# Optimization experiments

Measured on AMD Instinct MI355X. Metric: run time of the kernel, lower is better.

Reference implementation:

```python
import jax, jax.numpy as jnp
import numpy as np

# ---- config (from init_kwargs) ----
IMG_SIZE = (4096.0, 4096.0)
MAP_SIZE = (256, 256)
BASE_SIZE = 16
RATIOS = np.array([0.5, 1.0, 2.0], dtype=np.float64)
SCALES = np.array([8.0, 16.0, 32.0], dtype=np.float64)
FEAT_STRIDE = 16
RPN_MIN_SIZE = 16.0
PRE_NMS_N = 12000
POST_NMS_N = 2000
NMS_THRESH = 0.7


def _generate_anchors():
    base = np.array([1, 1, BASE_SIZE, BASE_SIZE], dtype=np.float64) - 1
    w = base[2] - base[0] + 1
    h = base[3] - base[1] + 1
    cx = base[0] + 0.5 * (w - 1)
    cy = base[1] + 0.5 * (h - 1)
    size = w * h
    ws = np.round(np.sqrt(size / RATIOS))
    hs = np.round(ws * RATIOS)
    ratio_anchors = np.stack([cx - 0.5 * (ws - 1), cy - 0.5 * (hs - 1),
                              cx + 0.5 * (ws - 1), cy + 0.5 * (hs - 1)], axis=1)
    out = []
    for a in ratio_anchors:
        aw = a[2] - a[0] + 1
        ah = a[3] - a[1] + 1
        acx = a[0] + 0.5 * (aw - 1)
        acy = a[1] + 0.5 * (ah - 1)
        ws2 = aw * SCALES
        hs2 = ah * SCALES
        out.append(np.stack([acx - 0.5 * (ws2 - 1), acy - 0.5 * (hs2 - 1),
                             acx + 0.5 * (ws2 - 1), acy + 0.5 * (hs2 - 1)], axis=1))
    return np.concatenate(out, axis=0).astype(np.float32)  # [A=9, 4]


def _all_anchors():
    A = _generate_anchors()
    H, W = MAP_SIZE
    sx = np.arange(W) * FEAT_STRIDE
    sy = np.arange(H) * FEAT_STRIDE
    sx, sy = np.meshgrid(sx, sy)
    shifts = np.stack([sx.ravel(), sy.ravel(), sx.ravel(), sy.ravel()], axis=1).astype(np.float32)  # [K,4]
    return (shifts[:, None, :] + A[None, :, :]).reshape(-1, 4)  # [K*A, 4]


_ALL_ANCHORS = _all_anchors()  # [N, 4] constant


def setup_inputs() -> dict:
    key = jax.random.key(0)
    k1, k2 = jax.random.split(key)
    n = _ALL_ANCHORS.shape[0]
    delta = jax.random.normal(k1, (1, n, 4), dtype=jnp.float32) * 0.1
    score = jax.random.uniform(k2, (1, n, 2), dtype=jnp.float32)
    return {"delta": delta, "score": score}


def _proposal_forward(delta, score):
    anchors = jnp.asarray(_ALL_ANCHORS)  # [N,4]
    d = delta[0]                         # [N,4]
    s = score[0, :, 1]                   # [N]

    widths = anchors[:, 2] - anchors[:, 0] + 1.0
    heights = anchors[:, 3] - anchors[:, 1] + 1.0
    ctr_x = anchors[:, 0] + 0.5 * widths
    ctr_y = anchors[:, 1] + 0.5 * heights
    pcx = d[:, 0] * widths + ctr_x
    pcy = d[:, 1] * heights + ctr_y
    pw = jnp.exp(d[:, 2]) * widths
    ph = jnp.exp(d[:, 3]) * heights
    x0 = jnp.clip(pcx - 0.5 * pw, 0.0, IMG_SIZE[0])
    y0 = jnp.clip(pcy - 0.5 * ph, 0.0, IMG_SIZE[1])
    x1 = jnp.clip(pcx + 0.5 * pw, 0.0, IMG_SIZE[0])
    y1 = jnp.clip(pcy + 0.5 * ph, 0.0, IMG_SIZE[1])
    props = jnp.stack([x0, y0, x1, y1], axis=1)  # [N,4]

    # min-size filter: mask instead of dynamic gather (jit-friendly)
    w = props[:, 2] - props[:, 0]
    h = props[:, 3] - props[:, 1]
    valid = (w >= RPN_MIN_SIZE) & (h >= RPN_MIN_SIZE)
    s = jnp.where(valid, s, -jnp.inf)

    top_s, top_i = jax.lax.top_k(s, PRE_NMS_N)   # sorted descending
    boxes = props[top_i]                          # [PRE,4]

    # greedy NMS over score-sorted boxes, fixed POST_NMS_N iterations
    areas = (boxes[:, 2] - boxes[:, 0]) * (boxes[:, 3] - boxes[:, 1])
    alive0 = top_s > -jnp.inf

    def step(alive, _):
        i = jnp.argmax(jnp.where(alive, top_s, -jnp.inf))
        ok = alive[i]
        b = boxes[i]
        xx0 = jnp.maximum(b[0], boxes[:, 0])
        yy0 = jnp.maximum(b[1], boxes[:, 1])
        xx1 = jnp.minimum(b[2], boxes[:, 2])
        yy1 = jnp.minimum(b[3], boxes[:, 3])
        inter = jnp.maximum(xx1 - xx0, 0.0) * jnp.maximum(yy1 - yy0, 0.0)
        iou = inter / jnp.maximum(areas[i] + areas - inter, 1e-8)
        alive = alive & (iou <= NMS_THRESH)
        out = jnp.where(ok, b, jnp.zeros_like(b))  # zero-pad like tf.pad
        return alive, out

    _, selected = jax.lax.scan(step, alive0, None, length=POST_NMS_N)  # [POST,4]
    return selected[None]  # [1, POST_NMS_N, 4]


def reference(delta, score):
    return _proposal_forward(delta, score)
```

## Files before the change

kernel.cpp:

```cpp
#include <hip/hip_runtime.h>
#include <hip/hip_bf16.h>

#define N_ANCH   589824
#define NBLK     2304
#define TOPK     12000
#define KPAD     12032
#define NW       188
#define OUTN     2000
#define CAP      32768

typedef unsigned long long u64;

__constant__ float c_aw[9] = {184.f, 368.f, 736.f, 128.f, 256.f, 512.f,  88.f, 176.f, 352.f};
__constant__ float c_ah[9] = { 96.f, 192.f, 384.f, 128.f, 256.f, 512.f, 176.f, 352.f, 704.f};

__device__ __forceinline__ void decode_one(int i, const float4* __restrict__ delta,
                                           float4* box, bool* valid) {
#pragma clang fp contract(off)
    int a    = i % 9;
    int cell = i / 9;
    int gx = cell & 255;
    int gy = cell >> 8;
    float w = c_aw[a], h = c_ah[a];
    float cx = (float)gx * 16.0f + 8.0f;
    float cy = (float)gy * 16.0f + 8.0f;
    float4 d = delta[i];
    float pcx = d.x * w + cx;
    float pcy = d.y * h + cy;
    float pw  = expf(d.z) * w;
    float ph  = expf(d.w) * h;
    float x0 = fminf(fmaxf(pcx - 0.5f * pw, 0.f), 4096.f);
    float y0 = fminf(fmaxf(pcy - 0.5f * ph, 0.f), 4096.f);
    float x1 = fminf(fmaxf(pcx + 0.5f * pw, 0.f), 4096.f);
    float y1 = fminf(fmaxf(pcy + 0.5f * ph, 0.f), 4096.f);
    *box = make_float4(x0, y0, x1, y1);
    *valid = (x1 - x0 >= 16.f) && (y1 - y0 >= 16.f);
}

__global__ __launch_bounds__(256) void k_score(const float4* __restrict__ delta,
                                               const float2* __restrict__ score,
                                               unsigned* __restrict__ ukey,
                                               unsigned* __restrict__ hist1) {
    __shared__ unsigned lh[256];
    int tid = threadIdx.x;
    lh[tid] = 0u;
    __syncthreads();
    int i = blockIdx.x * 256 + tid;
    float4 box; bool valid;
    decode_one(i, delta, &box, &valid);
    unsigned u = 0u;
    if (valid) {
        unsigned b = __float_as_uint(score[i].y);
        u = (b & 0x80000000u) ? ~b : (b | 0x80000000u);
    }
    ukey[i] = u;
    atomicAdd(&lh[u >> 24], 1u);
    __syncthreads();
    unsigned c = lh[tid];
    if (c) atomicAdd(&hist1[tid], c);
}

__global__ __launch_bounds__(256) void k_hist2(const unsigned* __restrict__ ukey,
                                               const unsigned* __restrict__ hist1,
                                               unsigned* __restrict__ hist2) {
    __shared__ unsigned ss[256];
    __shared__ unsigned lh[256];
    __shared__ unsigned s_b1;
    int tid = threadIdx.x;
    ss[tid] = hist1[tid];
    lh[tid] = 0u;
    if (tid == 0) s_b1 = 0u;
    __syncthreads();
    for (int d = 1; d < 256; d <<= 1) {
        unsigned v = (tid + d < 256) ? ss[tid + d] : 0u;
        __syncthreads();
        ss[tid] += v;
        __syncthreads();
    }
    if (ss[tid] >= (unsigned)TOPK && (tid == 255 || ss[tid + 1] < (unsigned)TOPK))
        s_b1 = (unsigned)tid;
    __syncthreads();
    unsigned b1 = s_b1;
    int i = blockIdx.x * 256 + tid;
    unsigned u = ukey[i];
    if ((u >> 24) == b1) atomicAdd(&lh[(u >> 16) & 255u], 1u);
    __syncthreads();
    unsigned c = lh[tid];
    if (c) atomicAdd(&hist2[tid], c);
}

__global__ __launch_bounds__(256) void k_compact(const unsigned* __restrict__ ukey,
                                                 const unsigned* __restrict__ hist1,
                                                 const unsigned* __restrict__ hist2,
                                                 unsigned* __restrict__ cnt,
                                                 u64* __restrict__ cand) {
    __shared__ unsigned ss[256];
    __shared__ unsigned s_b1, s_ab1, s_P;
    int tid = threadIdx.x;
    ss[tid] = hist1[tid];
    if (tid == 0) { s_b1 = 0u; s_ab1 = 0u; }
    __syncthreads();
    for (int d = 1; d < 256; d <<= 1) {
        unsigned v = (tid + d < 256) ? ss[tid + d] : 0u;
        __syncthreads();
        ss[tid] += v;
        __syncthreads();
    }
    if (ss[tid] >= (unsigned)TOPK && (tid == 255 || ss[tid + 1] < (unsigned)TOPK)) {
        s_b1 = (unsigned)tid;
        s_ab1 = (tid == 255) ? 0u : ss[tid + 1];
    }
    __syncthreads();
    unsigned b1 = s_b1, ab1 = s_ab1;
    ss[tid] = hist2[tid];
    if (tid == 0) s_P = (b1 << 8);
    __syncthreads();
    for (int d = 1; d < 256; d <<= 1) {
        unsigned v = (tid + d < 256) ? ss[tid + d] : 0u;
        __syncthreads();
        ss[tid] += v;
        __syncthreads();
    }
    unsigned target = (unsigned)TOPK - ab1;
    if (ss[tid] >= target && (tid == 255 || ss[tid + 1] < target))
        s_P = (b1 << 8) | (unsigned)tid;
    __syncthreads();
    unsigned P = s_P;

    int i = blockIdx.x * 256 + tid;
    unsigned u = ukey[i];
    bool pred = (u != 0u) && ((u >> 16) >= P);
    u64 m = __ballot(pred);
    if (m == 0ull) return;
    int lane = tid & 63;
    int leader = __ffsll(m) - 1;
    unsigned base = 0;
    if (lane == leader) base = atomicAdd(cnt, (unsigned)__popcll(m));
    base = __shfl(base, leader);
    if (pred) {
        u64 below = m & ((1ull << lane) - 1ull);
        unsigned pos = base + (unsigned)__popcll(below);
        if (pos < CAP) cand[pos] = ((u64)u << 32) | (unsigned)(~i);
    }
}

__global__ __launch_bounds__(256) void k_rankdec(const u64* __restrict__ cand,
                                                 const unsigned* __restrict__ ctrl,
                                                 const float4* __restrict__ delta,
                                                 float4* __restrict__ sboxes) {
    unsigned cnt = ctrl[3];
    int C = (int)(cnt < (unsigned)CAP ? cnt : (unsigned)CAP);
    if ((int)(blockIdx.x * 256) >= C) return;
    int t = blockIdx.x * 256 + threadIdx.x;
    u64 mykey = (t < C) ? cand[t] : ~0ull;
    int rank = 0;
    __shared__ u64 tile[256];
    for (int j0 = 0; j0 < C; j0 += 256) {
        int j = j0 + threadIdx.x;
        tile[threadIdx.x] = (j < C) ? cand[j] : 0ull;
        __syncthreads();
        int lim = (C - j0 < 256) ? (C - j0) : 256;
        #pragma unroll 4
        for (int jj = 0; jj < lim; ++jj) rank += (tile[jj] > mykey) ? 1 : 0;
        __syncthreads();
    }
    if (t < C && rank < TOPK) {
        int idx = (int)(~(unsigned)mykey);
        float4 box; bool v;
        decode_one(idx, delta, &box, &v);
        sboxes[rank] = box;
    }
}

__global__ __launch_bounds__(64) void k_mask(const float4* __restrict__ sboxes,
                                             u64* __restrict__ mcol) {
    int rb = blockIdx.y;
    int cb0 = blockIdx.x * 4;
    if (cb0 + 3 < rb) return;
    int tid = threadIdx.x;
    int r = rb * 64 + tid;
    float4 me = sboxes[r];
    float areaMe = (me.z - me.x) * (me.w - me.y);
    __shared__ float4 cbox[64];
    for (int q = 0; q < 4; ++q) {
        int cb = cb0 + q;
        if (cb < rb) continue;
        __syncthreads();
        cbox[tid] = sboxes[cb * 64 + tid];
        __syncthreads();
        u64 bits = 0ull;
        for (int j = 0; j < 64; ++j) {
            float4 o = cbox[j];
            float xx0 = fmaxf(me.x, o.x);
            float yy0 = fmaxf(me.y, o.y);
            float xx1 = fminf(me.z, o.z);
            float yy1 = fminf(me.w, o.w);
            float iw = fmaxf(xx1 - xx0, 0.f);
            float ih = fmaxf(yy1 - yy0, 0.f);
            float inter = iw * ih;
            float areaO = (o.z - o.x) * (o.w - o.y);
            float denom = fmaxf(areaMe + areaO - inter, 1e-8f);
            float iou = inter / denom;
            if (iou > 0.7f && (cb * 64 + j) != r) bits |= (1ull << j);
        }
        mcol[(size_t)cb * KPAD + r] = bits;
    }
}

__global__ __launch_bounds__(256) void k_reduce(const float4* __restrict__ sboxes,
                                                const unsigned* __restrict__ ctrl,
                                                const u64* __restrict__ mcol,
                                                float4* __restrict__ out) {
    int t = threadIdx.x;
    int lane = t & 63;
    int wave = t >> 6;
    unsigned cnt = ctrl[3];
    int C = (int)(cnt < (unsigned)CAP ? cnt : (unsigned)CAP);
    int nvalid = C < TOPK ? C : TOPK;
    int nblocks = (nvalid + 63) >> 6;

    __shared__ u64 s_rw[2];

    u64 removed_t = ~0ull;
    if (t < NW) {
        long long lo = (long long)t * 64;
        if (lo + 64 <= (long long)nvalid) removed_t = 0ull;
        else if (lo < (long long)nvalid)
            removed_t = ~((1ull << (unsigned)(nvalid - lo)) - 1ull);
    }

    int nk = 0;
    u64 p0=0,p1=0,p2=0,p3=0,p4=0,p5=0,p6=0,p7=0;
    u64 p8=0,p9=0,p10=0,p11=0,p12=0,p13=0,p14=0,p15=0;
    u64 dgnext = 0ull;
    if (nblocks > 0) dgnext = mcol[(size_t)0 * KPAD + lane];

    for (int b = 0; b < nblocks; ++b) {
        removed_t |= ((p0|p1)|(p2|p3)) | ((p4|p5)|(p6|p7));
        removed_t |= ((p8|p9)|(p10|p11)) | ((p12|p13)|(p14|p15));
        p0=p1=p2=p3=p4=p5=p6=p7=0ull;
        p8=p9=p10=p11=p12=p13=p14=p15=0ull;
        u64 dg = dgnext;
        if (t == b) s_rw[b & 1] = removed_t;
        __syncthreads();
        u64 rw = s_rw[b & 1];
        if (b + 1 < nblocks)
            dgnext = mcol[(size_t)(b + 1) * KPAD + (size_t)(b + 1) * 64 + lane];

        bool alive = ((rw >> lane) & 1ull) == 0ull;
        int budget = OUTN - nk;
        u64 keptmask = 0ull;
        int kc = 0;
        while (kc < budget) {
            u64 m = __ballot(alive);
            if (!m) break;
            int j = __ffsll(m) - 1;
            keptmask |= (1ull << j);
            ++kc;
            alive = alive && (lane != j) && (((dg >> j) & 1ull) == 0ull);
        }

        if (wave == 0 && ((keptmask >> lane) & 1ull)) {
            int pos = nk + (int)__popcll(keptmask & ((1ull << lane) - 1ull));
            out[pos] = sboxes[b * 64 + lane];
        }
        nk += kc;
        if (nk >= OUTN) break;

        if (kc > 0 && t > b && t < NW) {
            const u64* colp = mcol + (size_t)t * KPAD + (size_t)b * 64;
            u64 km = keptmask;
            int jf = __ffsll(km) - 1;
            int i0 = jf;                          km &= km - 1;
            int i1  = km ? __ffsll(km) - 1 : jf;  km &= km - 1;
            int i2  = km ? __ffsll(km) - 1 : jf;  km &= km - 1;
            int i3  = km ? __ffsll(km) - 1 : jf;  km &= km - 1;
            int i4  = km ? __ffsll(km) - 1 : jf;  km &= km - 1;
            int i5  = km ? __ffsll(km) - 1 : jf;  km &= km - 1;
            int i6  = km ? __ffsll(km) - 1 : jf;  km &= km - 1;
            int i7  = km ? __ffsll(km) - 1 : jf;  km &= km - 1;
            int i8  = km ? __ffsll(km) - 1 : jf;  km &= km - 1;
            int i9  = km ? __ffsll(km) - 1 : jf;  km &= km - 1;
            int i10 = km ? __ffsll(km) - 1 : jf;  km &= km - 1;
            int i11 = km ? __ffsll(km) - 1 : jf;  km &= km - 1;
            int i12 = km ? __ffsll(km) - 1 : jf;  km &= km - 1;
            int i13 = km ? __ffsll(km) - 1 : jf;  km &= km - 1;
            int i14 = km ? __ffsll(km) - 1 : jf;  km &= km - 1;
            int i15 = km ? __ffsll(km) - 1 : jf;  km &= km - 1;
            p0 = colp[i0];   p1 = colp[i1];   p2 = colp[i2];   p3 = colp[i3];
            p4 = colp[i4];   p5 = colp[i5];   p6 = colp[i6];   p7 = colp[i7];
            p8 = colp[i8];   p9 = colp[i9];   p10 = colp[i10]; p11 = colp[i11];
            p12 = colp[i12]; p13 = colp[i13]; p14 = colp[i14]; p15 = colp[i15];
            while (km) {
                int j = __ffsll(km) - 1; km &= km - 1;
                removed_t |= colp[j];
            }
        }
    }

    float4 z = make_float4(0.f, 0.f, 0.f, 0.f);
    for (int p = nk + t; p < OUTN; p += 256) out[p] = z;
}

extern "C" void kernel_launch(void* const* d_in, const int* in_sizes, int n_in,
                              void* d_out, int out_size, void* d_ws, size_t ws_size,
                              hipStream_t stream) {
    const float4* delta = (const float4*)d_in[0];
    const float2* score = (const float2*)d_in[1];
    char* ws = (char*)d_ws;

    unsigned* ukey  = (unsigned*)(ws + 0);
    u64*      cand  = (u64*)(ws + 2359296);
    unsigned* hist1 = (unsigned*)(ws + 2621440);
    unsigned* hist2 = (unsigned*)(ws + 2622464);
    unsigned* ctrl  = (unsigned*)(ws + 2623488);
    float4*   sbox  = (float4*)(ws + 2623552);
    u64*      mcol  = (u64*)(ws + 2816064);

    hipMemsetAsync(ws + 2621440, 0, 194624, stream);

    k_score  <<<NBLK,    256, 0, stream>>>(delta, score, ukey, hist1);
    k_hist2  <<<NBLK,    256, 0, stream>>>(ukey, hist1, hist2);
    k_compact<<<NBLK,    256, 0, stream>>>(ukey, hist1, hist2, ctrl + 3, cand);
    k_rankdec<<<CAP/256, 256, 0, stream>>>(cand, ctrl, delta, sbox);
    dim3 mgrid(47, NW);
    k_mask   <<<mgrid,   64,  0, stream>>>(sbox, mcol);
    k_reduce <<<1,       256, 0, stream>>>(sbox, ctrl, mcol, (float4*)d_out);
}
```

Before: 891.0 us.

## Single-pass 8192-bin histogram select, row-major mask, and pipelined NMS reduce

The two-level radix histogram (hist1 plus hist2) is replaced by a single 13-bit histogram accumulated in shared memory over grid-stride loops, which removes one full pass over the keys. The NMS mask is stored row-major with separate diagonal and superdiagonal arrays, and padded boxes are zeroed. The serial reduce now double-buffers the suppression-row loads and applies superdiagonal suppression through shared memory, aiming to shorten its critical path. In exchange, the 32 KB shared histogram may limit occupancy, and the row-major mask gathers are strided across threads.

```diff
diff --git a/kernel.cpp b/kernel.cpp
--- a/kernel.cpp
+++ b/kernel.cpp
@@ -1,13 +1,12 @@
 #include <hip/hip_runtime.h>
-#include <hip/hip_bf16.h>
 
 #define N_ANCH   589824
-#define NBLK     2304
 #define TOPK     12000
 #define KPAD     12032
 #define NW       188
 #define OUTN     2000
 #define CAP      32768
+#define NBIN     8192
 
 typedef unsigned long long u64;
 
@@ -40,36 +39,46 @@
 __global__ __launch_bounds__(256) void k_score(const float4* __restrict__ delta,
                                                const float2* __restrict__ score,
                                                unsigned* __restrict__ ukey,
-                                               unsigned* __restrict__ hist1) {
-    __shared__ unsigned lh[256];
+                                               unsigned* __restrict__ hist) {
+    __shared__ unsigned lh[NBIN];
     int tid = threadIdx.x;
-    lh[tid] = 0u;
+    for (int k = tid; k < NBIN; k += 256) lh[k] = 0u;
     __syncthreads();
-    int i = blockIdx.x * 256 + tid;
-    float4 box; bool valid;
-    decode_one(i, delta, &box, &valid);
-    unsigned u = 0u;
-    if (valid) {
-        unsigned b = __float_as_uint(score[i].y);
-        u = (b & 0x80000000u) ? ~b : (b | 0x80000000u);
-    }
-    ukey[i] = u;
-    atomicAdd(&lh[u >> 24], 1u);
+    for (int i = blockIdx.x * 256 + tid; i < N_ANCH; i += gridDim.x * 256) {
+        float4 box; bool valid;
+        decode_one(i, delta, &box, &valid);
+        unsigned u = 0u;
+        if (valid) {
+            unsigned b = __float_as_uint(score[i].y);
+            u = (b & 0x80000000u) ? ~b : (b | 0x80000000u);
+        }
+        ukey[i] = u;
+        atomicAdd(&lh[u >> 19], 1u);
+    }
     __syncthreads();
-    unsigned c = lh[tid];
-    if (c) atomicAdd(&hist1[tid], c);
-}
-
-__global__ __launch_bounds__(256) void k_hist2(const unsigned* __restrict__ ukey,
-                                               const unsigned* __restrict__ hist1,
-                                               unsigned* __restrict__ hist2) {
+    for (int k = tid; k < NBIN; k += 256) {
+        unsigned c = lh[k];
+        if (c) atomicAdd(&hist[k], c);
+    }
+}
+
+__global__ __launch_bounds__(256) void k_compact(const unsigned* __restrict__ ukey,
+                                                 const unsigned* __restrict__ hist,
+                                                 unsigned* __restrict__ cnt,
+                                                 u64* __restrict__ cand) {
     __shared__ unsigned ss[256];
-    __shared__ unsigned lh[256];
-    __shared__ unsigned s_b1;
+    __shared__ unsigned s_B;
     int tid = threadIdx.x;
-    ss[tid] = hist1[tid];
-    lh[tid] = 0u;
-    if (tid == 0) s_b1 = 0u;
+    int lane = tid & 63;
+    const uint4* hb = (const uint4*)hist + tid * 8;
+    unsigned cs = 0;
+    #pragma unroll
+    for (int k = 0; k < 8; ++k) {
+        uint4 h = hb[k];
+        cs += h.x + h.y + h.z + h.w;
+    }
+    ss[tid] = cs;
+    if (tid == 0) s_B = 0u;
     __syncthreads();
     for (int d = 1; d < 256; d <<= 1) {
         unsigned v = (tid + d < 256) ? ss[tid + d] : 0u;
@@ -77,70 +86,32 @@
         ss[tid] += v;
         __syncthreads();
     }
-    if (ss[tid] >= (unsigned)TOPK && (tid == 255 || ss[tid + 1] < (unsigned)TOPK))
-        s_b1 = (unsigned)tid;
+    if (ss[tid] >= (unsigned)TOPK && (tid == 255 || ss[tid + 1] < (unsigned)TOPK)) {
+        unsigned acc = (tid == 255) ? 0u : ss[tid + 1];
+        unsigned B = (unsigned)(tid * 32);
+        for (int j = 31; j >= 0; --j) {
+            acc += hist[tid * 32 + j];
+            if (acc >= (unsigned)TOPK) { B = (unsigned)(tid * 32 + j); break; }
+        }
+        s_B = B;
+    }
     __syncthreads();
-    unsigned b1 = s_b1;
-    int i = blockIdx.x * 256 + tid;
-    unsigned u = ukey[i];
-    if ((u >> 24) == b1) atomicAdd(&lh[(u >> 16) & 255u], 1u);
-    __syncthreads();
-    unsigned c = lh[tid];
-    if (c) atomicAdd(&hist2[tid], c);
-}
-
-__global__ __launch_bounds__(256) void k_compact(const unsigned* __restrict__ ukey,
-                                                 const unsigned* __restrict__ hist1,
-                                                 const unsigned* __restrict__ hist2,
-                                                 unsigned* __restrict__ cnt,
-                                                 u64* __restrict__ cand) {
-    __shared__ unsigned ss[256];
-    __shared__ unsigned s_b1, s_ab1, s_P;
-    int tid = threadIdx.x;
-    ss[tid] = hist1[tid];
-    if (tid == 0) { s_b1 = 0u; s_ab1 = 0u; }
-    __syncthreads();
-    for (int d = 1; d < 256; d <<= 1) {
-        unsigned v = (tid + d < 256) ? ss[tid + d] : 0u;
-        __syncthreads();
-        ss[tid] += v;
-        __syncthreads();
-    }
-    if (ss[tid] >= (unsigned)TOPK && (tid == 255 || ss[tid + 1] < (unsigned)TOPK)) {
-        s_b1 = (unsigned)tid;
-        s_ab1 = (tid == 255) ? 0u : ss[tid + 1];
-    }
-    __syncthreads();
-    unsigned b1 = s_b1, ab1 = s_ab1;
-    ss[tid] = hist2[tid];
-    if (tid == 0) s_P = (b1 << 8);
-    __syncthreads();
-    for (int d = 1; d < 256; d <<= 1) {
-        unsigned v = (tid + d < 256) ? ss[tid + d] : 0u;
-        __syncthreads();
-        ss[tid] += v;
-        __syncthreads();
-    }
-    unsigned target = (unsigned)TOPK - ab1;
-    if (ss[tid] >= target && (tid == 255 || ss[tid + 1] < target))
-        s_P = (b1 << 8) | (unsigned)tid;
-    __syncthreads();
-    unsigned P = s_P;
-
-    int i = blockIdx.x * 256 + tid;
-    unsigned u = ukey[i];
-    bool pred = (u != 0u) && ((u >> 16) >= P);
-    u64 m = __ballot(pred);
-    if (m == 0ull) return;
-    int lane = tid & 63;
-    int leader = __ffsll(m) - 1;
-    unsigned base = 0;
-    if (lane == leader) base = atomicAdd(cnt, (unsigned)__popcll(m));
-    base = __shfl(base, leader);
-    if (pred) {
-        u64 below = m & ((1ull << lane) - 1ull);
-        unsigned pos = base + (unsigned)__popcll(below);
-        if (pos < CAP) cand[pos] = ((u64)u << 32) | (unsigned)(~i);
+    unsigned B = s_B;
+    for (int i = blockIdx.x * 256 + tid; i < N_ANCH; i += gridDim.x * 256) {
+        unsigned u = ukey[i];
+        bool pred = (u != 0u) && ((u >> 19) >= B);
+        u64 m = __ballot(pred);
+        if (m) {
+            int leader = __ffsll(m) - 1;
+            unsigned base = 0;
+            if (lane == leader) base = atomicAdd(cnt, (unsigned)__popcll(m));
+            base = __shfl(base, leader);
+            if (pred) {
+                u64 below = m & ((1ull << lane) - 1ull);
+                unsigned pos = base + (unsigned)__popcll(below);
+                if (pos < CAP) cand[pos] = ((u64)u << 32) | (unsigned)(~i);
+            }
+        }
     }
 }
 
@@ -150,8 +121,10 @@
                                                  float4* __restrict__ sboxes) {
     unsigned cnt = ctrl[3];
     int C = (int)(cnt < (unsigned)CAP ? cnt : (unsigned)CAP);
+    int nv = C < TOPK ? C : TOPK;
+    int t = blockIdx.x * 256 + threadIdx.x;
+    if (t >= nv && t < KPAD) sboxes[t] = make_float4(0.f, 0.f, 0.f, 0.f);
     if ((int)(blockIdx.x * 256) >= C) return;
-    int t = blockIdx.x * 256 + threadIdx.x;
     u64 mykey = (t < C) ? cand[t] : ~0ull;
     int rank = 0;
     __shared__ u64 tile[256];
@@ -173,7 +146,8 @@
 }
 
 __global__ __launch_bounds__(64) void k_mask(const float4* __restrict__ sboxes,
-                                             u64* __restrict__ mcol) {
+                                             u64* __restrict__ mask,
+                                             u64* __restrict__ dgsd) {
     int rb = blockIdx.y;
     int cb0 = blockIdx.x * 4;
     if (cb0 + 3 < rb) return;
@@ -203,49 +177,105 @@
             float iou = inter / denom;
             if (iou > 0.7f && (cb * 64 + j) != r) bits |= (1ull << j);
         }
-        mcol[(size_t)cb * KPAD + r] = bits;
-    }
-}
+        mask[(size_t)r * NW + cb] = bits;
+        if (cb == rb)     dgsd[2 * r]     = bits;
+        if (cb == rb + 1) dgsd[2 * r + 1] = bits;
+    }
+}
+
+#define EXTRACT16()                                            \
+    u64 km = keptmask;                                         \
+    int jf = __ffsll(km) - 1;                                  \
+    int i0 = jf;                          km &= km - 1;        \
+    int i1  = km ? __ffsll(km) - 1 : jf;  km &= km - 1;        \
+    int i2  = km ? __ffsll(km) - 1 : jf;  km &= km - 1;        \
+    int i3  = km ? __ffsll(km) - 1 : jf;  km &= km - 1;        \
+    int i4  = km ? __ffsll(km) - 1 : jf;  km &= km - 1;        \
+    int i5  = km ? __ffsll(km) - 1 : jf;  km &= km - 1;        \
+    int i6  = km ? __ffsll(km) - 1 : jf;  km &= km - 1;        \
+    int i7  = km ? __ffsll(km) - 1 : jf;  km &= km - 1;        \
+    int i8  = km ? __ffsll(km) - 1 : jf;  km &= km - 1;        \
+    int i9  = km ? __ffsll(km) - 1 : jf;  km &= km - 1;        \
+    int i10 = km ? __ffsll(km) - 1 : jf;  km &= km - 1;        \
+    int i11 = km ? __ffsll(km) - 1 : jf;  km &= km - 1;        \
+    int i12 = km ? __ffsll(km) - 1 : jf;  km &= km - 1;        \
+    int i13 = km ? __ffsll(km) - 1 : jf;  km &= km - 1;        \
+    int i14 = km ? __ffsll(km) - 1 : jf;  km &= km - 1;        \
+    int i15 = km ? __ffsll(km) - 1 : jf;  km &= km - 1;
+
+#define ISSUE(P)                                               \
+    if (kc > 0 && tid > b + 1 && tid < NW) {                   \
+        const u64* mt2 = mask + (size_t)b * 64 * NW + tid;     \
+        P##0  = mt2[(size_t)i0  * NW];                         \
+        P##1  = mt2[(size_t)i1  * NW];                         \
+        P##2  = mt2[(size_t)i2  * NW];                         \
+        P##3  = mt2[(size_t)i3  * NW];                         \
+        P##4  = mt2[(size_t)i4  * NW];                         \
+        P##5  = mt2[(size_t)i5  * NW];                         \
+        P##6  = mt2[(size_t)i6  * NW];                         \
+        P##7  = mt2[(size_t)i7  * NW];                         \
+        P##8  = mt2[(size_t)i8  * NW];                         \
+        P##9  = mt2[(size_t)i9  * NW];                         \
+        P##10 = mt2[(size_t)i10 * NW];                         \
+        P##11 = mt2[(size_t)i11 * NW];                         \
+        P##12 = mt2[(size_t)i12 * NW];                         \
+        P##13 = mt2[(size_t)i13 * NW];                         \
+        P##14 = mt2[(size_t)i14 * NW];                         \
+        P##15 = mt2[(size_t)i15 * NW];                         \
+        while (km) {      \
+            int j = __ffsll(km) - 1; km &= km - 1;             \
+            removed_t |= mt2[(size_t)j * NW];                  \
+        }                                                      \
+    }
+
+#define FOLD(P)                                                           \
+    removed_t |= ((P##0|P##1)|(P##2|P##3)) | ((P##4|P##5)|(P##6|P##7));   \
+    removed_t |= ((P##8|P##9)|(P##10|P##11)) | ((P##12|P##13)|(P##14|P##15));
 
 __global__ __launch_bounds__(256) void k_reduce(const float4* __restrict__ sboxes,
                                                 const unsigned* __restrict__ ctrl,
-                                                const u64* __restrict__ mcol,
+                                                const u64* __restrict__ mask,
+                                                const u64* __restrict__ dgsd,
                                                 float4* __restrict__ out) {
-    int t = threadIdx.x;
-    int lane = t & 63;
-    int wave = t >> 6;
+    int tid = threadIdx.x;
+    int lane = tid & 63;
+    int wave = tid >> 6;
     unsigned cnt = ctrl[3];
     int C = (int)(cnt < (unsigned)CAP ? cnt : (unsigned)CAP);
-    int nvalid = C < TOPK ? C : TOPK;
-    int nblocks = (nvalid + 63) >> 6;
+    int nv = C < TOPK ? C : TOPK;
+    int nblocks = (nv + 63) >> 6;
 
     __shared__ u64 s_rw[2];
+    __shared__ u64 s_sup[4];
+    if (tid < 4) s_sup[tid] = 0ull;
 
     u64 removed_t = ~0ull;
-    if (t < NW) {
-        long long lo = (long long)t * 64;
-        if (lo + 64 <= (long long)nvalid) removed_t = 0ull;
-        else if (lo < (long long)nvalid)
-            removed_t = ~((1ull << (unsigned)(nvalid - lo)) - 1ull);
-    }
+    if (tid < NW) {
+        long long lo = (long long)tid * 64;
+        if (lo + 64 <= (long long)nv) removed_t = 0ull;
+        else if (lo < (long long)nv)
+            removed_t = ~((1ull << (unsigned)(nv - lo)) - 1ull);
+    }
+
+    u64 pA0=0,pA1=0,pA2=0,pA3=0,pA4=0,pA5=0,pA6=0,pA7=0;
+    u64 pA8=0,pA9=0,pA10=0,pA11=0,pA12=0,pA13=0,pA14=0,pA15=0;
+    u64 pB0=0,pB1=0,pB2=0,pB3=0,pB4=0,pB5=0,pB6=0,pB7=0;
+    u64 pB8=0,pB9=0,pB10=0,pB11=0,pB12=0,pB13=0,pB14=0,pB15=0;
+
+    const ulonglong2* D = (const ulonglong2*)dgsd;
+    ulonglong2 dsnext = make_ulonglong2(0ull, 0ull);
+    if (nblocks > 0) dsnext = D[lane];
 
     int nk = 0;
-    u64 p0=0,p1=0,p2=0,p3=0,p4=0,p5=0,p6=0,p7=0;
-    u64 p8=0,p9=0,p10=0,p11=0,p12=0,p13=0,p14=0,p15=0;
-    u64 dgnext = 0ull;
-    if (nblocks > 0) dgnext = mcol[(size_t)0 * KPAD + lane];
-
     for (int b = 0; b < nblocks; ++b) {
-        removed_t |= ((p0|p1)|(p2|p3)) | ((p4|p5)|(p6|p7));
-        removed_t |= ((p8|p9)|(p10|p11)) | ((p12|p13)|(p14|p15));
-        p0=p1=p2=p3=p4=p5=p6=p7=0ull;
-        p8=p9=p10=p11=p12=p13=p14=p15=0ull;
-        u64 dg = dgnext;
-        if (t == b) s_rw[b & 1] = removed_t;
-        __syncthreads();
-        u64 rw = s_rw[b & 1];
-        if (b + 1 < nblocks)
-            dgnext = mcol[(size_t)(b + 1) * KPAD + (size_t)(b + 1) * 64 + lane];
+        if ((b & 1) == 0) { FOLD(pA); } else { FOLD(pB); }
+        ulonglong2 ds = dsnext;
+        if (tid == b) s_rw[b & 1] = removed_t;
+        __syncthreads();
+        u64 rw = s_rw[b & 1] | s_sup[b & 3];
+        if (tid == 254) s_sup[(b + 2) & 3] = 0ull;
+        u64 dg = ds.x, sg = ds.y;
+        if (b + 1 < nblocks) dsnext = D[(b + 1) * 64 + lane];
 
         bool alive = ((rw >> lane) & 1ull) == 0ull;
         int budget = OUTN - nk;
@@ -263,43 +293,17 @@
         if (wave == 0 && ((keptmask >> lane) & 1ull)) {
             int pos = nk + (int)__popcll(keptmask & ((1ull << lane) - 1ull));
             out[pos] = sboxes[b * 64 + lane];
+            atomicOr(&s_sup[(b + 1) & 3], sg);
         }
         nk += kc;
         if (nk >= OUTN) break;
 
-        if (kc > 0 && t > b && t < NW) {
-            const u64* colp = mcol + (size_t)t * KPAD + (size_t)b * 64;
-            u64 km = keptmask;
-            int jf = __ffsll(km) - 1;
-            int i0 = jf;                          km &= km - 1;
-            int i1  = km ? __ffsll(km) - 1 : jf;  km &= km - 1;
-            int i2  = km ? __ffsll(km) - 1 : jf;  km &= km - 1;
-            int i3  = km ? __ffsll(km) - 1 : jf;  km &= km - 1;
-            int i4  = km ? __ffsll(km) - 1 : jf;  km &= km - 1;
-            int i5  = km ? __ffsll(km) - 1 : jf;  km &= km - 1;
-            int i6  = km ? __ffsll(km) - 1 : jf;  km &= km - 1;
-            int i7  = km ? __ffsll(km) - 1 : jf;  km &= km - 1;
-            int i8  = km ? __ffsll(km) - 1 : jf;  km &= km - 1;
-            int i9  = km ? __ffsll(km) - 1 : jf;  km &= km - 1;
-            int i10 = km ? __ffsll(km) - 1 : jf;  km &= km - 1;
-            int i11 = km ? __ffsll(km) - 1 : jf;  km &= km - 1;
-            int i12 = km ? __ffsll(km) - 1 : jf;  km &= km - 1;
-            int i13 = km ? __ffsll(km) - 1 : jf;  km &= km - 1;
-            int i14 = km ? __ffsll(km) - 1 : jf;  km &= km - 1;
-            int i15 = km ? __ffsll(km) - 1 : jf;  km &= km - 1;
-            p0 = colp[i0];   p1 = colp[i1];   p2 = colp[i2];   p3 = colp[i3];
-            p4 = colp[i4];   p5 = colp[i5];   p6 = colp[i6];   p7 = colp[i7];
-            p8 = colp[i8];   p9 = colp[i9];   p10 = colp[i10]; p11 = colp[i11];
-            p12 = colp[i12]; p13 = colp[i13]; p14 = colp[i14]; p15 = colp[i15];
-            while (km) {
-                int j = __ffsll(km) - 1; km &= km - 1;
-                removed_t |= colp[j];
-            }
-        }
+        EXTRACT16();
+        if ((b & 1) == 0) { ISSUE(pA); } else { ISSUE(pB); }
     }
 
     float4 z = make_float4(0.f, 0.f, 0.f, 0.f);
-    for (int p = nk + t; p < OUTN; p += 256) out[p] = z;
+    for (int p = nk + tid; p < OUTN; p += 256) out[p] = z;
 }
 
 extern "C" void kernel_launch(void* const* d_in, const int* in_sizes, int n_in,
@@ -309,21 +313,20 @@
     const float2* score = (const float2*)d_in[1];
     char* ws = (char*)d_ws;
 
-    unsigned* ukey  = (unsigned*)(ws + 0);
-    u64*      cand  = (u64*)(ws + 2359296);
-    unsigned* hist1 = (unsigned*)(ws + 2621440);
-    unsigned* hist2 = (unsigned*)(ws + 2622464);
-    unsigned* ctrl  = (unsigned*)(ws + 2623488);
-    float4*   sbox  = (float4*)(ws + 2623552);
-    u64*      mcol  = (u64*)(ws + 2816064);
-
-    hipMemsetAsync(ws + 2621440, 0, 194624, stream);
-
-    k_score  <<<NBLK,    256, 0, stream>>>(delta, score, ukey, hist1);
-    k_hist2  <<<NBLK,    256, 0, stream>>>(ukey, hist1, hist2);
-    k_compact<<<NBLK,    256, 0, stream>>>(ukey, hist1, hist2, ctrl + 3, cand);
+    unsigned* ukey = (unsigned*)(ws + 0);
+    u64*      cand = (u64*)(ws + 2359296);
+    unsigned* hist = (unsigned*)(ws + 2621440);
+    unsigned* ctrl = (unsigned*)(ws + 2654208);
+    float4*   sbox = (float4*)(ws + 2654272);
+    u64*      dgsd = (u64*)(ws + 2846784);
+    u64*      mask = (u64*)(ws + 3039296);
+
+    hipMemsetAsync(ws + 2621440, 0, 32832, stream);
+
+    k_score  <<<1024, 256, 0, stream>>>(delta, score, ukey, hist);
+    k_compact<<<1024, 256, 0, stream>>>(ukey, hist, ctrl + 3, cand);
     k_rankdec<<<CAP/256, 256, 0, stream>>>(cand, ctrl, delta, sbox);
     dim3 mgrid(47, NW);
-    k_mask   <<<mgrid,   64,  0, stream>>>(sbox, mcol);
-    k_reduce <<<1,       256, 0, stream>>>(sbox, ctrl, mcol, (float4*)d_out);
-}
+    k_mask   <<<mgrid, 64, 0, stream>>>(sbox, mask, dgsd);
+    k_reduce <<<1,    256, 0, stream>>>(sbox, ctrl, mask, dgsd, (float4*)d_out);
+}
```

Result: slower. 1.184 ms (+32.9%).
